# Performance work log

Measured on AMD Instinct MI355X. Metric: run time of the kernel, lower is better.

Reference implementation:

```python
import math
import jax, jax.numpy as jnp
import numpy as np

B, T, C = 1, 2048, 2048
H, G, D = 16, 4, 128          # n_head, n_query_groups, head_size; C == H*D
Q_PER_KV = H // G
EPS = 1e-5


def _apply_rope_interleaved(x, cos, sin):
    # x: [B, T, h, D]; cos/sin: [T, D//2]; interleaved (GPT-J) style pairs
    x1 = x[..., 0::2]
    x2 = x[..., 1::2]
    c = cos[None, :, None, :]
    s = sin[None, :, None, :]
    o1 = x1 * c - x2 * s
    o2 = x1 * s + x2 * c
    return jnp.stack([o1, o2], axis=-1).reshape(x.shape)


def setup_inputs() -> dict:
    key = jax.random.key(0)
    k0, k1, k2, k3 = jax.random.split(key, 4)
    x = jax.random.normal(k0, (B, T, C), jnp.float32)
    # rotary cache (standard theta=10000)
    inv_freq = 1.0 / (10000.0 ** (np.arange(0, D, 2, dtype=np.float64) / D))
    ang = np.outer(np.arange(T, dtype=np.float64), inv_freq)
    cos = jnp.asarray(np.cos(ang), jnp.float32)
    sin = jnp.asarray(np.sin(ang), jnp.float32)
    # RetNet per-head decay mask: D[h,i,j] = gamma_h^(i-j) for i>=j else 0
    gammas = 1.0 - 2.0 ** (-5.0 - np.arange(H, dtype=np.float64))
    i = np.arange(T)[:, None]
    j = np.arange(T)[None, :]
    diff = np.maximum(i - j, 0).astype(np.float64)
    m = np.where(i >= j, gammas[:, None, None] ** diff[None], 0.0)
    mask = jnp.asarray(m, jnp.float32)
    std = 0.02
    W_reten = jax.random.normal(k1, (C, (H + 2 * G) * D), jnp.float32) * std
    W_gate = jax.random.normal(k2, (C, C), jnp.float32) * std
    W_proj = jax.random.normal(k3, (C, C), jnp.float32) * std
    return {"x": x, "cos": cos, "sin": sin, "mask": mask,
            "W_reten": W_reten, "W_gate": W_gate, "W_proj": W_proj,
            "max_seq_length": T}


def reference(x, cos, sin, mask, W_reten, W_gate, W_proj, max_seq_length):
    # fused qkv projection, grouped-query layout
    qkv = (x @ W_reten).reshape(B, T, G, Q_PER_KV + 2, D)
    q = qkv[..., :Q_PER_KV, :].reshape(B, T, H, D)
    k = qkv[..., Q_PER_KV:Q_PER_KV + 1, :].reshape(B, T, G, D)
    v = qkv[..., Q_PER_KV + 1:, :].reshape(B, T, G, D)
    q = _apply_rope_interleaved(q, cos, sin)
    k = _apply_rope_interleaved(k, cos, sin)
    # [B, h, T, D]
    q = q.transpose(0, 2, 1, 3)
    k = jnp.repeat(k.transpose(0, 2, 1, 3), Q_PER_KV, axis=1)
    v = jnp.repeat(v.transpose(0, 2, 1, 3), Q_PER_KV, axis=1)
    # parallel retention: masked (decay) scores, no softmax
    scale = 1.0 / math.sqrt(D)
    qk = jnp.einsum('bhtd,bhsd->bhts', q, k) * scale
    qk = qk * mask[None]
    y = jnp.einsum('bhts,bhsd->bhtd', qk, v)
    # group norm = RMSNorm (no weight) over head_size
    y = y.transpose(0, 2, 1, 3)  # [B, T, H, D]
    y = y * jax.lax.rsqrt(jnp.mean(y * y, axis=-1, keepdims=True) + EPS)
    y = y.reshape(B, T, C)
    g = jax.nn.silu(x @ W_gate)
    return (g * y) @ W_proj
```

## Files before the change

kernel.cpp:

```cpp
#include <hip/hip_runtime.h>
#include <hip/hip_bf16.h>
#include <cstdint>
#include <cstddef>

typedef __bf16 bf16x8 __attribute__((ext_vector_type(8)));
typedef __bf16 bf16x4 __attribute__((ext_vector_type(4)));
typedef __bf16 bf16x2 __attribute__((ext_vector_type(2)));
typedef float  f32x4  __attribute__((ext_vector_type(4)));
typedef float  f32x2  __attribute__((ext_vector_type(2)));

#define T_SEQ 2048
#define CDIM  2048
#define NH    16
#define NG    4
#define DH    128
#define NCHUNK 32

__device__ __forceinline__ void gl_lds16(const __bf16* g, __bf16* l) {
  __builtin_amdgcn_global_load_lds(
      (const __attribute__((address_space(1))) void*)g,
      (__attribute__((address_space(3))) void*)l, 16, 0, 0);
}

__global__ __launch_bounds__(256) void pre_kernel(
    const float* __restrict__ x, const float* __restrict__ Wr,
    const float* __restrict__ Wg, const float* __restrict__ Wp,
    __bf16* __restrict__ xb, __bf16* __restrict__ wtb, __bf16* __restrict__ wpb) {
  __shared__ __bf16 tile[64][68];
  int bid = blockIdx.x;
  int tid = threadIdx.x;
  if (bid < 2048) {
    size_t i = ((size_t)bid * 256 + tid) * 8;
    f32x4 a = *(const f32x4*)(x + i);
    f32x4 b = *(const f32x4*)(x + i + 4);
    bf16x8 o;
#pragma unroll
    for (int j = 0; j < 4; ++j) { o[j] = (__bf16)a[j]; o[4 + j] = (__bf16)b[j]; }
    *(bf16x8*)(xb + i) = o;
    return;
  }
  int rel = bid - 2048;
  const float* W; __bf16* Wt; int N;
  if (rel < 1536)      { W = Wr; Wt = wtb;                        N = 3072; }
  else if (rel < 2560) { W = Wg; Wt = wtb + (size_t)3072 * CDIM;  N = 2048; rel -= 1536; }
  else                 { W = Wp; Wt = wpb;                        N = 2048; rel -= 2560; }
  const int K = 2048;
  int k0 = (rel & 31) * 64, n0 = (rel >> 5) * 64;
  int c4 = (tid & 15) * 4, r = tid >> 4;
#pragma unroll
  for (int rr = 0; rr < 4; ++rr) {
    int row = r + rr * 16;
    f32x4 v = *(const f32x4*)(W + (size_t)(k0 + row) * N + n0 + c4);
#pragma unroll
    for (int j = 0; j < 4; ++j) tile[row][c4 + j] = (__bf16)v[j];
  }
  __syncthreads();
  int n = tid >> 2, seg = tid & 3;
  __bf16 vals[16];
#pragma unroll
  for (int j = 0; j < 16; ++j) vals[j] = tile[seg * 16 + j][n];
  __bf16* dst = Wt + (size_t)(n0 + n) * K + k0 + seg * 16;
  *(bf16x8*)(dst)     = *(bf16x8*)(&vals[0]);
  *(bf16x8*)(dst + 8) = *(bf16x8*)(&vals[8]);
}

__global__ __launch_bounds__(256) void ropekt_kernel(const float* __restrict__ qkv,
    const float* __restrict__ cosb, const float* __restrict__ sinb,
    __bf16* __restrict__ qb, __bf16* __restrict__ kb,
    __bf16* __restrict__ vtb, __bf16* __restrict__ ktb) {
  __shared__ __bf16 vt[64][136];
  int bid = blockIdx.x;
  int tid = threadIdx.x;
  if (bid < 2048) {
    int t = bid;
    int w = tid >> 6, l = tid & 63;
    float c = cosb[t * 64 + l], s = sinb[t * 64 + l];
#pragma unroll
    for (int it = 0; it < 5; ++it) {
      int slot = w + it * 4;
      int g = slot / 5, j = slot % 5;
      const float* src = qkv + (size_t)t * 3072 + g * 768 + j * 128;
      f32x2 xv = *(const f32x2*)(src + 2 * l);
      bf16x2 o;
      o[0] = (__bf16)(xv[0] * c - xv[1] * s);
      o[1] = (__bf16)(xv[0] * s + xv[1] * c);
      __bf16* dst = (j < 4) ? (qb + ((size_t)(g * 4 + j) * T_SEQ + t) * DH)
                            : (kb + ((size_t)g * T_SEQ + t) * DH);
      *(bf16x2*)(dst + 2 * l) = o;
    }
    return;
  }
  if (bid < 2176) {
    int rel = bid - 2048;
    int g = rel >> 5, t0 = (rel & 31) * 64;
#pragma unroll
    for (int it = 0; it < 8; ++it) {
      int q = it * 256 + tid;
      int tt = q >> 5, dq = q & 31;
      f32x4 v = *(const f32x4*)(qkv + (size_t)(t0 + tt) * 3072 + g * 768 + 640 + dq * 4);
#pragma unroll
      for (int j = 0; j < 4; ++j) vt[tt][dq * 4 + j] = (__bf16)v[j];
    }
    __syncthreads();
    int d = tid >> 1, half = tid & 1;
    __bf16 outv[32];
#pragma unroll
    for (int j = 0; j < 32; ++j) outv[j] = vt[half * 32 + j][d];
    __bf16* dst = vtb + ((size_t)g * DH + d) * T_SEQ + t0 + half * 32;
#pragma unroll
    for (int q4 = 0; q4 < 4; ++q4) *(bf16x8*)(dst + q4 * 8) = *(bf16x8*)(&outv[q4 * 8]);
    return;
  }
  int rel = bid - 2176;
  int g = rel >> 5, t0 = (rel & 31) * 64;
#pragma unroll
  for (int it = 0; it < 8; ++it) {
    int q = it * 256 + tid;
    int tt = q >> 5, dq = q & 31;
    int t = t0 + tt;
    f32x4 v = *(const f32x4*)(qkv + (size_t)t * 3072 + g * 768 + 512 + dq * 4);
    float c0 = cosb[t * 64 + dq * 2],     s0 = sinb[t * 64 + dq * 2];
    float c1 = cosb[t * 64 + dq * 2 + 1], s1 = sinb[t * 64 + dq * 2 + 1];
    vt[tt][dq * 4 + 0] = (__bf16)(v[0] * c0 - v[1] * s0);
    vt[tt][dq * 4 + 1] = (__bf16)(v[0] * s0 + v[1] * c0);
    vt[tt][dq * 4 + 2] = (__bf16)(v[2] * c1 - v[3] * s1);
    vt[tt][dq * 4 + 3] = (__bf16)(v[2] * s1 + v[3] * c1);
  }
  __syncthreads();
  int d = tid >> 1, half = tid & 1;
  __bf16 outv[32];
#pragma unroll
  for (int j = 0; j < 32; ++j) outv[j] = vt[half * 32 + j][d];
  __bf16* dst = ktb + ((size_t)g * DH + d) * T_SEQ + t0 + half * 32;
#pragma unroll
  for (int q4 = 0; q4 < 4; ++q4) *(bf16x8*)(dst + q4 * 8) = *(bf16x8*)(&outv[q4 * 8]);
}

__global__ __launch_bounds__(256) void uscan_kernel(const __bf16* __restrict__ vtb,
                                                    const __bf16* __restrict__ ktb,
                                                    __bf16* __restrict__ St) {
  int bid = blockIdx.x;
  int h = bid >> 4, m = (bid >> 1) & 7, half = bid & 1;
  int g = h >> 2;
  int tid = threadIdx.x, w = tid >> 6, l = tid & 63, lr = l & 15, lg = l >> 4;
  int jf = half * 4 + w;
  float l2g = log2f(1.0f - exp2f(-5.0f - (float)h));
  float ginv = exp2f(-l2g);
  float df   = exp2f(l2g * 64.0f);
  float wk[2];
#pragma unroll
  for (int kk = 0; kk < 2; ++kk) wk[kk] = exp2f(l2g * (float)(64 - (kk * 32 + lg * 8)));
  const __bf16* vrow = vtb + ((size_t)g * DH + m * 16 + lr) * T_SEQ;
  const __bf16* krow = ktb + ((size_t)g * DH + jf * 16 + lr) * T_SEQ;
  f32x4 S = {0.f, 0.f, 0.f, 0.f};
  for (int c = 0; c < NCHUNK; ++c) {
    f32x4 u = {0.f, 0.f, 0.f, 0.f};
#pragma unroll
    for (int kk = 0; kk < 2; ++kk) {
      int j0 = c * 64 + kk * 32 + lg * 8;
      bf16x8 av = *(const bf16x8*)(vrow + j0);
      bf16x8 bv = *(const bf16x8*)(krow + j0);
      bf16x8 aw;
      float wj = wk[kk];
#pragma unroll
      for (int jj = 0; jj < 8; ++jj) { aw[jj] = (__bf16)((float)av[jj] * wj); wj *= ginv; }
      u = __builtin_amdgcn_mfma_f32_16x16x32_bf16(aw, bv, u, 0, 0, 0);
    }
    __bf16* out = St + ((size_t)(h * NCHUNK + c) * 128 + m * 16 + lg * 4) * 128 + jf * 16 + lr;
#pragma unroll
    for (int r = 0; r < 4; ++r) out[r * 128] = (__bf16)S[r];
#pragma unroll
    for (int r = 0; r < 4; ++r) S[r] = df * S[r] + u[r];
  }
}

__global__ __launch_bounds__(256) void attn2_kernel(const __bf16* __restrict__ qb,
    const __bf16* __restrict__ kb, const __bf16* __restrict__ vtb,
    const __bf16* __restrict__ St, const __bf16* __restrict__ gateb,
    __bf16* __restrict__ ynormb) {
  __shared__ __bf16 kl[64 * 128];
  __shared__ __bf16 vl[128 * 64];
  __shared__ __bf16 pl[4][16 * 64];
  int h = blockIdx.x >> 5, qt = blockIdx.x & 31;
  int g = h >> 2;
  int w = threadIdx.x >> 6, l = threadIdx.x & 63;
  int lr = l & 15, lg = l >> 4;
  int t0b = qt * 64;
  int t0 = t0b + w * 16;
  bf16x8 qf[4];
#pragma unroll
  for (int kbk = 0; kbk < 4; ++kbk)
    qf[kbk] = *(const bf16x8*)(qb + ((size_t)h * T_SEQ + t0 + lr) * DH + kbk * 32 + lg * 8);
  float gamma = 1.0f - exp2f(-5.0f - (float)h);
  float l2g = log2f(gamma);
  const float scale = 0.088388347648318447f;
  int s0 = t0b;
#pragma unroll
  for (int it = 0; it < 4; ++it) {
    int fg = it * 256 + threadIdx.x;
    {
      int ss = fg >> 4, gr = fg & 15;
      bf16x8 kv = *(const bf16x8*)(kb + ((size_t)g * T_SEQ + s0 + ss) * DH + gr * 8);
      *(bf16x8*)((char*)kl + ss * 256 + ((gr * 16) ^ ((ss & 7) << 4))) = kv;
    }
    {
      int d = fg >> 3, gv = fg & 7;
      bf16x8 vv = *(const bf16x8*)(vtb + ((size_t)g * DH + d) * T_SEQ + s0 + gv * 8);
      *(bf16x8*)((char*)vl + d * 128 + ((gv * 16) ^ ((d & 7) << 4))) = vv;
    }
  }
  float wfac = scale * exp2f(l2g * (float)(w * 16 + lr));
  bf16x8 qwf[4];
#pragma unroll
  for (int kbk = 0; kbk < 4; ++kbk)
#pragma unroll
    for (int e = 0; e < 8; ++e) qwf[kbk][e] = (__bf16)((float)qf[kbk][e] * wfac);
  f32x4 acc[8] = {};
  const __bf16* Sb = St + (size_t)(h * NCHUNK + qt) * 16384;
#pragma unroll
  for (int dc = 0; dc < 8; ++dc)
#pragma unroll
    for (int kc = 0; kc < 4; ++kc) {
      bf16x8 sf = *(const bf16x8*)(Sb + (dc * 16 + lr) * 128 + kc * 32 + lg * 8);
      acc[dc] = __builtin_amdgcn_mfma_f32_16x16x32_bf16(qwf[kc], sf, acc[dc], 0, 0, 0);
    }
  __syncthreads();
#pragma unroll
  for (int sc = 0; sc < 4; ++sc) {
    f32x4 p = {0.f, 0.f, 0.f, 0.f};
    int srow = sc * 16 + lr;
#pragma unroll
    for (int kbk = 0; kbk < 4; ++kbk) {
      bf16x8 kf = *(const bf16x8*)((char*)kl + srow * 256 +
                                   ((kbk * 64 + lg * 16) ^ ((srow & 7) << 4)));
      p = __builtin_amdgcn_mfma_f32_16x16x32_bf16(qf[kbk], kf, p, 0, 0, 0);
    }
#pragma unroll
    for (int r = 0; r < 4; ++r) {
      int tl = lg * 4 + r;
      int diff = (w * 16 + tl) - srow;
      float val = 0.0f;
      if (diff >= 0) val = p[r] * scale * exp2f((float)diff * l2g);
      *(__bf16*)((char*)(pl[w]) + tl * 128 +
                 (((sc * 16 + lr) * 2) ^ ((tl & 7) << 4))) = (__bf16)val;
    }
  }
  bf16x8 pa[2];
#pragma unroll
  for (int kc = 0; kc < 2; ++kc)
    pa[kc] = *(const bf16x8*)((char*)(pl[w]) + lr * 128 +
                              ((kc * 64 + lg * 16) ^ ((lr & 7) << 4)));
#pragma unroll
  for (int dc = 0; dc < 8; ++dc) {
#pragma unroll
    for (int kc = 0; kc < 2; ++kc) {
      int vrow = dc * 16 + lr;
      bf16x8 vf = *(const bf16x8*)((char*)vl + vrow * 128 +
                                   ((kc * 64 + lg * 16) ^ ((vrow & 7) << 4)));
      acc[dc] = __builtin_amdgcn_mfma_f32_16x16x32_bf16(pa[kc], vf, acc[dc], 0, 0, 0);
    }
  }
  float rs[4];
#pragma unroll
  for (int r = 0; r < 4; ++r) {
    float ssum = 0.f;
#pragma unroll
    for (int dc = 0; dc < 8; ++dc) ssum += acc[dc][r] * acc[dc][r];
    ssum += __shfl_xor(ssum, 1, 64);
    ssum += __shfl_xor(ssum, 2, 64);
    ssum += __shfl_xor(ssum, 4, 64);
    ssum += __shfl_xor(ssum, 8, 64);
    rs[r] = rsqrtf(ssum * (1.0f / 128.0f) + 1e-5f);
  }
#pragma unroll
  for (int dc = 0; dc < 8; ++dc)
#pragma unroll
    for (int r = 0; r < 4; ++r) {
      size_t idx = (size_t)(t0 + lg * 4 + r) * CDIM + h * DH + dc * 16 + lr;
      float gv = (float)gateb[idx];
      ynormb[idx] = (__bf16)(acc[dc][r] * rs[r] * gv);
    }
}

template<int MODE>
__global__ __launch_bounds__(256) void gemm_gl_kernel(
    const __bf16* __restrict__ A, const __bf16* __restrict__ Bt,
    float* __restrict__ Cf, __bf16* __restrict__ Cg, int M, int N, int K) {
  __shared__ __bf16 Asb[64 * 64];
  __shared__ __bf16 Bsb[128 * 64];
  int m0 = blockIdx.x * 64, n0 = blockIdx.y * 128;
  int tid = threadIdx.x;
  int w = tid >> 6, l = tid & 63;
  int wr = w >> 1, wc = w & 1;
  int lr = l & 15, lg = l >> 4;
  int nk = K >> 6;
  const __bf16* Ab = A + (size_t)m0 * K;
  const __bf16* Bb = Bt + (size_t)n0 * K;
  f32x4 acc[2][4] = {};
  for (int kt = 0; kt < nk; ++kt) {
    int k0 = kt << 6;
#pragma unroll
    for (int c = 0; c < 2; ++c) {
      int ca = c * 256 + tid;
      int row = ca >> 3, kseg = ca & 7;
      gl_lds16(Ab + (size_t)row * K + k0 + ((kseg ^ (row & 7)) << 3), Asb + ca * 8);
    }
#pragma unroll
    for (int c = 0; c < 4; ++c) {
      int cb = c * 256 + tid;
      int row = cb >> 3, kseg = cb & 7;
      gl_lds16(Bb + (size_t)row * K + k0 + ((kseg ^ (row & 7)) << 3), Bsb + cb * 8);
    }
    __syncthreads();
    bf16x8 av[2][2], bv[4][2];
#pragma unroll
    for (int i = 0; i < 2; ++i)
#pragma unroll
      for (int kk = 0; kk < 2; ++kk) {
        int row = wr * 32 + i * 16 + lr;
        av[i][kk] = *(const bf16x8*)((const char*)Asb +
            ((row * 128 + kk * 64 + lg * 16) ^ ((lr & 7) << 4)));
      }
#pragma unroll
    for (int j = 0; j < 4; ++j)
#pragma unroll
      for (int kk = 0; kk < 2; ++kk) {
        int row = wc * 64 + j * 16 + lr;
        bv[j][kk] = *(const bf16x8*)((const char*)Bsb +
            ((row * 128 + kk * 64 + lg * 16) ^ ((lr & 7) << 4)));
      }
#pragma unroll
    for (int kk = 0; kk < 2; ++kk)
#pragma unroll
      for (int i = 0; i < 2; ++i)
#pragma unroll
        for (int j = 0; j < 4; ++j)
          acc[i][j] = __builtin_amdgcn_mfma_f32_16x16x32_bf16(av[i][kk], bv[j][kk],
                                                              acc[i][j], 0, 0, 0);
    __syncthreads();
  }
#pragma unroll
  for (int i = 0; i < 2; ++i) {
    int row = m0 + wr * 32 + i * 16 + lg * 4;
#pragma unroll
    for (int j = 0; j < 4; ++j) {
      int col = n0 + wc * 64 + j * 16 + lr;
#pragma unroll
      for (int r = 0; r < 4; ++r) {
        float z = acc[i][j][r];
        if (MODE == 0) {
          Cf[(size_t)(row + r) * N + col] = z;
        } else {
          if (n0 < 3072) {
            Cf[(size_t)(row + r) * 3072 + col] = z;
          } else {
            float sv = z / (1.0f + expf(-z));
            Cg[(size_t)(row + r) * 2048 + (col - 3072)] = (__bf16)sv;
          }
        }
      }
    }
  }
}

extern "C" void kernel_launch(void* const* d_in, const int* in_sizes, int n_in,
                              void* d_out, int out_size, void* d_ws, size_t ws_size,
                              hipStream_t stream) {
  const float* x    = (const float*)d_in[0];
  const float* cosb = (const float*)d_in[1];
  const float* sinb = (const float*)d_in[2];
  const float* Wr   = (const float*)d_in[4];
  const float* Wg   = (const float*)d_in[5];
  const float* Wp   = (const float*)d_in[6];

  char* ws = (char*)d_ws;
  size_t off = 0;
  auto alloc = [&](size_t bytes) { void* p = ws + off; off += (bytes + 255) & ~(size_t)255; return p; };
  __bf16* xb     = (__bf16*)alloc((size_t)CDIM * CDIM * 2);
  __bf16* wtb    = (__bf16*)alloc((size_t)5120 * CDIM * 2);
  __bf16* wpb    = (__bf16*)alloc((size_t)CDIM * CDIM * 2);
  char*   qkvblk = (char*)  alloc((size_t)T_SEQ * 3072 * 4);
  __bf16* qb     = (__bf16*)alloc((size_t)NH * T_SEQ * DH * 2);
  __bf16* kbp    = (__bf16*)alloc((size_t)NG * T_SEQ * DH * 2);
  __bf16* vtb    = (__bf16*)alloc((size_t)NG * DH * T_SEQ * 2);
  __bf16* ktb    = (__bf16*)alloc((size_t)NG * DH * T_SEQ * 2);
  __bf16* gateb  = (__bf16*)alloc((size_t)CDIM * CDIM * 2);
  __bf16* Stb    = (__bf16*)alloc((size_t)NH * NCHUNK * 128 * 128 * 2);
  float*  qkv    = (float*)qkvblk;
  __bf16* ynormb = (__bf16*)qkvblk;

  pre_kernel<<<5632, 256, 0, stream>>>(x, Wr, Wg, Wp, xb, wtb, wpb);
  gemm_gl_kernel<1><<<dim3(32, 40), 256, 0, stream>>>(xb, wtb, qkv, gateb, 2048, 5120, 2048);
  ropekt_kernel<<<2048 + NG * 32 * 2, 256, 0, stream>>>(qkv, cosb, sinb, qb, kbp, vtb, ktb);
  uscan_kernel<<<256, 256, 0, stream>>>(vtb, ktb, Stb);
  attn2_kernel<<<NH * NCHUNK, 256, 0, stream>>>(qb, kbp, vtb, Stb, gateb, ynormb);
  gemm_gl_kernel<0><<<dim3(32, 16), 256, 0, stream>>>(ynormb, wpb, (float*)d_out, nullptr,
                                                      2048, 2048, 2048);
}
```

Before: 172.0 us.

## Fuse RoPE and K/V transpose into QKV GEMM epilogue, drop ropekt kernel

```diff
diff --git a/kernel.cpp b/kernel.cpp
--- a/kernel.cpp
+++ b/kernel.cpp
@@ -62,78 +62,6 @@
   __bf16* dst = Wt + (size_t)(n0 + n) * K + k0 + seg * 16;
   *(bf16x8*)(dst)     = *(bf16x8*)(&vals[0]);
   *(bf16x8*)(dst + 8) = *(bf16x8*)(&vals[8]);
-}
-
-__global__ __launch_bounds__(256) void ropekt_kernel(const float* __restrict__ qkv,
-    const float* __restrict__ cosb, const float* __restrict__ sinb,
-    __bf16* __restrict__ qb, __bf16* __restrict__ kb,
-    __bf16* __restrict__ vtb, __bf16* __restrict__ ktb) {
-  __shared__ __bf16 vt[64][136];
-  int bid = blockIdx.x;
-  int tid = threadIdx.x;
-  if (bid < 2048) {
-    int t = bid;
-    int w = tid >> 6, l = tid & 63;
-    float c = cosb[t * 64 + l], s = sinb[t * 64 + l];
-#pragma unroll
-    for (int it = 0; it < 5; ++it) {
-      int slot = w + it * 4;
-      int g = slot / 5, j = slot % 5;
-      const float* src = qkv + (size_t)t * 3072 + g * 768 + j * 128;
-      f32x2 xv = *(const f32x2*)(src + 2 * l);
-      bf16x2 o;
-      o[0] = (__bf16)(xv[0] * c - xv[1] * s);
-      o[1] = (__bf16)(xv[0] * s + xv[1] * c);
-      __bf16* dst = (j < 4) ? (qb + ((size_t)(g * 4 + j) * T_SEQ + t) * DH)
-                            : (kb + ((size_t)g * T_SEQ + t) * DH);
-      *(bf16x2*)(dst + 2 * l) = o;
-    }
-    return;
-  }
-  if (bid < 2176) {
-    int rel = bid - 2048;
-    int g = rel >> 5, t0 = (rel & 31) * 64;
-#pragma unroll
-    for (int it = 0; it < 8; ++it) {
-      int q = it * 256 + tid;
-      int tt = q >> 5, dq = q & 31;
-      f32x4 v = *(const f32x4*)(qkv + (size_t)(t0 + tt) * 3072 + g * 768 + 640 + dq * 4);
-#pragma unroll
-      for (int j = 0; j < 4; ++j) vt[tt][dq * 4 + j] = (__bf16)v[j];
-    }
-    __syncthreads();
-    int d = tid >> 1, half = tid & 1;
-    __bf16 outv[32];
-#pragma unroll
-    for (int j = 0; j < 32; ++j) outv[j] = vt[half * 32 + j][d];
-    __bf16* dst = vtb + ((size_t)g * DH + d) * T_SEQ + t0 + half * 32;
-#pragma unroll
-    for (int q4 = 0; q4 < 4; ++q4) *(bf16x8*)(dst + q4 * 8) = *(bf16x8*)(&outv[q4 * 8]);
-    return;
-  }
-  int rel = bid - 2176;
-  int g = rel >> 5, t0 = (rel & 31) * 64;
-#pragma unroll
-  for (int it = 0; it < 8; ++it) {
-    int q = it * 256 + tid;
-    int tt = q >> 5, dq = q & 31;
-    int t = t0 + tt;
-    f32x4 v = *(const f32x4*)(qkv + (size_t)t * 3072 + g * 768 + 512 + dq * 4);
-    float c0 = cosb[t * 64 + dq * 2],     s0 = sinb[t * 64 + dq * 2];
-    float c1 = cosb[t * 64 + dq * 2 + 1], s1 = sinb[t * 64 + dq * 2 + 1];
-    vt[tt][dq * 4 + 0] = (__bf16)(v[0] * c0 - v[1] * s0);
-    vt[tt][dq * 4 + 1] = (__bf16)(v[0] * s0 + v[1] * c0);
-    vt[tt][dq * 4 + 2] = (__bf16)(v[2] * c1 - v[3] * s1);
-    vt[tt][dq * 4 + 3] = (__bf16)(v[2] * s1 + v[3] * c1);
-  }
-  __syncthreads();
-  int d = tid >> 1, half = tid & 1;
-  __bf16 outv[32];
-#pragma unroll
-  for (int j = 0; j < 32; ++j) outv[j] = vt[half * 32 + j][d];
-  __bf16* dst = ktb + ((size_t)g * DH + d) * T_SEQ + t0 + half * 32;
-#pragma unroll
-  for (int q4 = 0; q4 < 4; ++q4) *(bf16x8*)(dst + q4 * 8) = *(bf16x8*)(&outv[q4 * 8]);
 }
 
 __global__ __launch_bounds__(256) void uscan_kernel(const __bf16* __restrict__ vtb,
@@ -285,7 +213,11 @@
 template<int MODE>
 __global__ __launch_bounds__(256) void gemm_gl_kernel(
     const __bf16* __restrict__ A, const __bf16* __restrict__ Bt,
-    float* __restrict__ Cf, __bf16* __restrict__ Cg, int M, int N, int K) {
+    float* __restrict__ Cf, __bf16* __restrict__ Cg,
+    const float* __restrict__ cosb, const float* __restrict__ sinb,
+    __bf16* __restrict__ qb, __bf16* __restrict__ kb,
+    __bf16* __restrict__ vtb, __bf16* __restrict__ ktb,
+    int M, int N, int K) {
   __shared__ __bf16 Asb[64 * 64];
   __shared__ __bf16 Bsb[128 * 64];
   int m0 = blockIdx.x * 64, n0 = blockIdx.y * 128;
@@ -339,25 +271,79 @@
                                                               acc[i][j], 0, 0, 0);
     __syncthreads();
   }
+  if (MODE == 0) {
+#pragma unroll
+    for (int i = 0; i < 2; ++i) {
+      int row = m0 + wr * 32 + i * 16 + lg * 4;
+#pragma unroll
+      for (int j = 0; j < 4; ++j) {
+        int col = n0 + wc * 64 + j * 16 + lr;
+#pragma unroll
+        for (int r = 0; r < 4; ++r)
+          Cf[(size_t)(row + r) * N + col] = acc[i][j][r];
+      }
+    }
+    return;
+  }
+  if (n0 >= 3072) {
+#pragma unroll
+    for (int i = 0; i < 2; ++i) {
+      int row = m0 + wr * 32 + i * 16 + lg * 4;
+#pragma unroll
+      for (int j = 0; j < 4; ++j) {
+        int col = n0 + wc * 64 + j * 16 + lr;
+#pragma unroll
+        for (int r = 0; r < 4; ++r) {
+          float z = acc[i][j][r];
+          float sv = z / (1.0f + expf(-z));
+          Cg[(size_t)(row + r) * 2048 + (col - 3072)] = (__bf16)sv;
+        }
+      }
+    }
+    return;
+  }
 #pragma unroll
   for (int i = 0; i < 2; ++i) {
-    int row = m0 + wr * 32 + i * 16 + lg * 4;
+    int row0 = m0 + wr * 32 + i * 16 + lg * 4;
 #pragma unroll
     for (int j = 0; j < 4; ++j) {
-      int col = n0 + wc * 64 + j * 16 + lr;
-#pragma unroll
-      for (int r = 0; r < 4; ++r) {
-        float z = acc[i][j][r];
-        if (MODE == 0) {
-          Cf[(size_t)(row + r) * N + col] = z;
-        } else {
-          if (n0 < 3072) {
-            Cf[(size_t)(row + r) * 3072 + col] = z;
-          } else {
-            float sv = z / (1.0f + expf(-z));
-            Cg[(size_t)(row + r) * 2048 + (col - 3072)] = (__bf16)sv;
-          }
+      int cb = n0 + wc * 64 + j * 16;
+      int g = cb / 768, cm = cb % 768;
+      int dbase = (cm < 512) ? (cm & 127) : (cm < 640) ? (cm - 512) : (cm - 640);
+      int d = dbase + lr;
+      float ov[4];
+      if (cm < 640) {
+#pragma unroll
+        for (int r = 0; r < 4; ++r) {
+          float z = acc[i][j][r];
+          float pz = __shfl_xor(z, 1, 64);
+          int t = row0 + r;
+          float cc = cosb[t * 64 + (d >> 1)];
+          float ss = sinb[t * 64 + (d >> 1)];
+          ov[r] = (lr & 1) ? (pz * ss + z * cc) : (z * cc - pz * ss);
         }
+      } else {
+#pragma unroll
+        for (int r = 0; r < 4; ++r) ov[r] = acc[i][j][r];
+      }
+      if (cm < 512) {
+        int hh = g * 4 + (cm >> 7);
+#pragma unroll
+        for (int r = 0; r < 4; ++r)
+          qb[((size_t)hh * T_SEQ + row0 + r) * DH + d] = (__bf16)ov[r];
+      } else if (cm < 640) {
+        bf16x4 kv;
+#pragma unroll
+        for (int r = 0; r < 4; ++r) {
+          kv[r] = (__bf16)ov[r];
+          kb[((size_t)g * T_SEQ + row0 + r) * DH + d] = kv[r];
+        }
+        *(bf16x4*)(ktb + ((size_t)g * DH + d) * T_SEQ + row0) = kv;
+      } else {
+        bf16x4 vv;
+#pragma unroll
+        for (int r = 0; r < 4; ++r) vv[r] = (__bf16)ov[r];
+        *(bf16x4*)(vtb + ((size_t)g * DH + d) * T_SEQ + row0) = vv;
       }
     }
   }
@@ -379,21 +365,20 @@
   __bf16* xb     = (__bf16*)alloc((size_t)CDIM * CDIM * 2);
   __bf16* wtb    = (__bf16*)alloc((size_t)5120 * CDIM * 2);
   __bf16* wpb    = (__bf16*)alloc((size_t)CDIM * CDIM * 2);
-  char*   qkvblk = (char*)  alloc((size_t)T_SEQ * 3072 * 4);
   __bf16* qb     = (__bf16*)alloc((size_t)NH * T_SEQ * DH * 2);
   __bf16* kbp    = (__bf16*)alloc((size_t)NG * T_SEQ * DH * 2);
   __bf16* vtb    = (__bf16*)alloc((size_t)NG * DH * T_SEQ * 2);
   __bf16* ktb    = (__bf16*)alloc((size_t)NG * DH * T_SEQ * 2);
   __bf16* gateb  = (__bf16*)alloc((size_t)CDIM * CDIM * 2);
   __bf16* Stb    = (__bf16*)alloc((size_t)NH * NCHUNK * 128 * 128 * 2);
-  float*  qkv    = (float*)qkvblk;
-  __bf16* ynormb = (__bf16*)qkvblk;
+  __bf16* ynormb = (__bf16*)alloc((size_t)T_SEQ * CDIM * 2);
 
   pre_kernel<<<5632, 256, 0, stream>>>(x, Wr, Wg, Wp, xb, wtb, wpb);
-  gemm_gl_kernel<1><<<dim3(32, 40), 256, 0, stream>>>(xb, wtb, qkv, gateb, 2048, 5120, 2048);
-  ropekt_kernel<<<2048 + NG * 32 * 2, 256, 0, stream>>>(qkv, cosb, sinb, qb, kbp, vtb, ktb);
+  gemm_gl_kernel<1><<<dim3(32, 40), 256, 0, stream>>>(
+      xb, wtb, nullptr, gateb, cosb, sinb, qb, kbp, vtb, ktb, 2048, 5120, 2048);
   uscan_kernel<<<256, 256, 0, stream>>>(vtb, ktb, Stb);
   attn2_kernel<<<NH * NCHUNK, 256, 0, stream>>>(qb, kbp, vtb, Stb, gateb, ynormb);
-  gemm_gl_kernel<0><<<dim3(32, 16), 256, 0, stream>>>(ynormb, wpb, (float*)d_out, nullptr,
-                                                      2048, 2048, 2048);
-}
+  gemm_gl_kernel<0><<<dim3(32, 16), 256, 0, stream>>>(
+      ynormb, wpb, (float*)d_out, nullptr, nullptr, nullptr, nullptr, nullptr, nullptr, nullptr,
+      2048, 2048, 2048);
+}
```

Result: faster. 164.0 us (-4.6%).
